# Performance work log

Measured on AMD Instinct MI355X. Metric: run time of the kernel, lower is better.

Reference implementation:

```python
import jax, jax.numpy as jnp
import numpy as np

N_NODES = 35
N_EDGES = 1190
N_VIEWS = 6
C1_IN, C1_OUT = 1, 256
C2_IN, C2_OUT = 256, 256
C3_IN, C3_OUT = 256, 64


def _nnconv(x, edge_attr, src, dst, nn_w, nn_b, lin_w, bias, c_in, c_out):
    """PyG NNConv with aggr='mean': per-edge MLP weight, gather-matvec-scatter."""
    # per-edge weight matrices: [E, c_in, c_out]
    W = jax.nn.relu(edge_attr @ nn_w.T + nn_b).reshape(-1, c_in, c_out)
    # gather source features and apply per-edge weight: [E, c_out]
    msg = jnp.einsum('ei,eio->eo', x[src], W)
    # scatter-mean into target nodes
    agg = jax.ops.segment_sum(msg, dst, num_segments=N_NODES)
    cnt = jax.ops.segment_sum(jnp.ones((msg.shape[0],), msg.dtype), dst,
                              num_segments=N_NODES)
    agg = agg / jnp.maximum(cnt, 1.0)[:, None]
    # root transform (lin has no bias in PyG) + conv bias
    return agg + x @ lin_w.T + bias


def setup_inputs() -> dict:
    key = jax.random.key(0)
    ks = jax.random.split(key, 16)
    s = 0.05
    x = jnp.ones((N_NODES, C1_IN), jnp.float32)
    edge_attr = jax.random.uniform(ks[0], (N_EDGES, N_VIEWS), jnp.float32)
    edge_index = jax.random.randint(ks[1], (2, N_EDGES), 0, N_NODES, jnp.int32)
    inp = {
        'x': x, 'edge_attr': edge_attr, 'edge_index': edge_index,
        'nn1_w': jax.random.normal(ks[2], (C1_IN * C1_OUT, N_VIEWS), jnp.float32) * s,
        'nn1_b': jax.random.normal(ks[3], (C1_IN * C1_OUT,), jnp.float32) * s,
        'lin1_w': jax.random.normal(ks[4], (C1_OUT, C1_IN), jnp.float32) * s,
        'b1': jax.random.normal(ks[5], (C1_OUT,), jnp.float32) * s,
        'nn2_w': jax.random.normal(ks[6], (C2_IN * C2_OUT, N_VIEWS), jnp.float32) * s,
        'nn2_b': jax.random.normal(ks[7], (C2_IN * C2_OUT,), jnp.float32) * s,
        'lin2_w': jax.random.normal(ks[8], (C2_OUT, C2_IN), jnp.float32) * s,
        'b2': jax.random.normal(ks[9], (C2_OUT,), jnp.float32) * s,
        'nn3_w': jax.random.normal(ks[10], (C3_IN * C3_OUT, N_VIEWS), jnp.float32) * s,
        'nn3_b': jax.random.normal(ks[11], (C3_IN * C3_OUT,), jnp.float32) * s,
        'lin3_w': jax.random.normal(ks[12], (C3_OUT, C3_IN), jnp.float32) * s,
        'b3': jax.random.normal(ks[13], (C3_OUT,), jnp.float32) * s,
    }
    return inp


def reference(x, edge_attr, edge_index, nn1_w, nn1_b, lin1_w, b1,
              nn2_w, nn2_b, lin2_w, b2, nn3_w, nn3_b, lin3_w, b3):
    src, dst = edge_index[0], edge_index[1]
    x = jax.nn.relu(_nnconv(x, edge_attr, src, dst, nn1_w, nn1_b, lin1_w, b1, C1_IN, C1_OUT))
    x = jax.nn.relu(_nnconv(x, edge_attr, src, dst, nn2_w, nn2_b, lin2_w, b2, C2_IN, C2_OUT))
    x = jax.nn.relu(_nnconv(x, edge_attr, src, dst, nn3_w, nn3_b, lin3_w, b3, C3_IN, C3_OUT))
    # CBT: pairwise L1 distances over feature dim -> [N, N]
    # (equivalent to repeat(35,1,1) / transpose / abs / sum since N == 35)
    cbt = jnp.abs(x[None, :, :] - x[:, None, :]).sum(-1)
    return cbt
```

## Files before the change

### kernel.cpp

```cpp
#include <hip/hip_runtime.h>


#define NN 35
#define NE 1190
#define MAXE 80

#define OFF_CNT  0
#define OFF_EL   64
#define OFF_X1   2944
#define OFF_X2   11904
#define OFF_X3   20864
#define OFF_AGG3 23168

__global__ __launch_bounds__(512) void x1_k(
    float* __restrict__ ws, const float* __restrict__ x,
    const float* __restrict__ ea, const int* __restrict__ ei,
    const float* __restrict__ w1, const float* __restrict__ b1w,
    const float* __restrict__ lin1, const float* __restrict__ b1) {
    __shared__ int elistS[MAXE];
    __shared__ int ecntS;
    __shared__ float partS[8 * 64];
    const int tid = threadIdx.x, bid = blockIdx.x;
    if (bid >= 140) {
        const int idx = (bid - 140) * 512 + tid;
        if (idx < NN * 64) ws[OFF_AGG3 + idx] = 0.f;
        return;
    }
    const int n = bid >> 2, och = bid & 3;
    if (tid == 0) ecntS = 0;
    __syncthreads();
    for (int e = tid; e < NE; e += 512) {
        if (ei[NE + e] == n) {
            const int p = atomicAdd(&ecntS, 1);
            if (p < MAXE) elistS[p] = e;
        }
    }
    __syncthreads();
    const int deg = ecntS;
    const int dl = deg < MAXE ? deg : MAXE;
    const int ol = tid & 63, ech = tid >> 6;
    const int o = och * 64 + ol;
    const float2* wr = (const float2*)(w1 + o * 6);
    const float2 wv0 = wr[0], wv1 = wr[1], wv2 = wr[2];
    const float bb = b1w[o];
    float a = 0.f;
    for (int k = ech; k < dl; k += 8) {
        const int e = elistS[k];
        const float2* eap = (const float2*)(ea + e * 6);
        const float2 a0 = eap[0], a1 = eap[1], a2 = eap[2];
        float d = bb;
        d = fmaf(a0.x, wv0.x, d); d = fmaf(a0.y, wv0.y, d);
        d = fmaf(a1.x, wv1.x, d); d = fmaf(a1.y, wv1.y, d);
        d = fmaf(a2.x, wv2.x, d); d = fmaf(a2.y, wv2.y, d);
        a = fmaf(x[ei[e]], fmaxf(d, 0.f), a);
    }
    partS[ech * 64 + ol] = a;
    __syncthreads();
    if (ech == 0) {
        float s = a;
#pragma unroll
        for (int p = 1; p < 8; p++) s += partS[p * 64 + ol];
        const float c = fmaxf((float)deg, 1.f);
        ws[OFF_X1 + n * 256 + o] = fmaxf(s / c + x[n] * lin1[o] + b1[o], 0.f);
    }
    if (och == 0) {
        if (tid < dl) ((int*)(ws + OFF_EL))[n * MAXE + tid] = elistS[tid];
        if (tid == 0) ws[OFF_CNT + n] = (float)deg;
    }
}

__global__ __launch_bounds__(512) void x2_k(
    float* __restrict__ ws, const float* __restrict__ ea,
    const int* __restrict__ ei, const float* __restrict__ w2,
    const float* __restrict__ b2w, const float* __restrict__ lin2,
    const float* __restrict__ b2) {
    __shared__ float smem[11264];
    float* xsS = smem;
    float* x1S = smem + 10240;
    float* easS = smem + 10496;
    int* srcS = (int*)(smem + 10976);
    int* elS = (int*)(smem + 11056);
    float* partA = smem;
    float* partB = smem + 512;
    __shared__ float cS;
    const int tid = threadIdx.x;
    const int n = blockIdx.x >> 4, og = blockIdx.x & 15;
    const int ol = tid & 15, ic = tid >> 4;
    const int o = og * 16 + ol;
    if (tid == 0) cS = ws[OFF_CNT + n];
    if (tid < MAXE) elS[tid] = ((const int*)(ws + OFF_EL))[n * MAXE + tid];
    if (tid >= 448) {
        const int q = tid - 448;
        *(float4*)&x1S[q * 4] = *(const float4*)(ws + OFF_X1 + n * 256 + q * 4);
    }
    __syncthreads();
    const int deg = (int)cS;
    const int dl = deg < MAXE ? deg : MAXE;
    if (tid < dl) {
        const int eid = elS[tid];
        srcS[tid] = ei[eid];
        const float2* eap = (const float2*)(ea + eid * 6);
        *(float2*)&easS[tid * 6] = eap[0];
        *(float2*)&easS[tid * 6 + 2] = eap[1];
        *(float2*)&easS[tid * 6 + 4] = eap[2];
    }
    float accm = 0.f;
    for (int p = 0; p < 2; ++p) {
        __syncthreads();
        for (int idx = tid; idx < dl * 32; idx += 512) {
            const int e = idx >> 5, ip = (idx & 31) * 4;
            *(float4*)&xsS[e * 128 + ip] =
                *(const float4*)(ws + OFF_X1 + srcS[e] * 256 + p * 128 + ip);
        }
        __syncthreads();
        const int i0 = p * 128 + ic * 4;
        const float* wp0 = w2 + (size_t)((i0 + 0) * 256 + o) * 6;
        const float* wp1 = w2 + (size_t)((i0 + 1) * 256 + o) * 6;
        const float* wp2 = w2 + (size_t)((i0 + 2) * 256 + o) * 6;
        const float* wp3 = w2 + (size_t)((i0 + 3) * 256 + o) * 6;
        const float2 wa0 = *(const float2*)wp0;
        const float2 wb0 = *(const float2*)(wp0 + 2);
        const float2 wc0 = *(const float2*)(wp0 + 4);
        const float2 wa1 = *(const float2*)wp1;
        const float2 wb1 = *(const float2*)(wp1 + 2);
        const float2 wc1 = *(const float2*)(wp1 + 4);
        const float2 wa2 = *(const float2*)wp2;
        const float2 wb2 = *(const float2*)(wp2 + 2);
        const float2 wc2 = *(const float2*)(wp2 + 4);
        const float2 wa3 = *(const float2*)wp3;
        const float2 wb3 = *(const float2*)(wp3 + 2);
        const float2 wc3 = *(const float2*)(wp3 + 4);
        const float bb0 = b2w[(i0 + 0) * 256 + o];
        const float bb1 = b2w[(i0 + 1) * 256 + o];
        const float bb2 = b2w[(i0 + 2) * 256 + o];
        const float bb3 = b2w[(i0 + 3) * 256 + o];
        for (int e = 0; e < dl; ++e) {
            const float2 e01 = *(const float2*)&easS[e * 6];
            const float2 e23 = *(const float2*)&easS[e * 6 + 2];
            const float2 e45 = *(const float2*)&easS[e * 6 + 4];
            const float4 xv = *(const float4*)&xsS[e * 128 + ic * 4];
            float d0 = bb0, d1 = bb1, d2 = bb2, d3 = bb3;
            d0 = fmaf(e01.x, wa0.x, d0); d1 = fmaf(e01.x, wa1.x, d1);
            d2 = fmaf(e01.x, wa2.x, d2); d3 = fmaf(e01.x, wa3.x, d3);
            d0 = fmaf(e01.y, wa0.y, d0); d1 = fmaf(e01.y, wa1.y, d1);
            d2 = fmaf(e01.y, wa2.y, d2); d3 = fmaf(e01.y, wa3.y, d3);
            d0 = fmaf(e23.x, wb0.x, d0); d1 = fmaf(e23.x, wb1.x, d1);
            d2 = fmaf(e23.x, wb2.x, d2); d3 = fmaf(e23.x, wb3.x, d3);
            d0 = fmaf(e23.y, wb0.y, d0); d1 = fmaf(e23.y, wb1.y, d1);
            d2 = fmaf(e23.y, wb2.y, d2); d3 = fmaf(e23.y, wb3.y, d3);
            d0 = fmaf(e45.x, wc0.x, d0); d1 = fmaf(e45.x, wc1.x, d1);
            d2 = fmaf(e45.x, wc2.x, d2); d3 = fmaf(e45.x, wc3.x, d3);
            d0 = fmaf(e45.y, wc0.y, d0); d1 = fmaf(e45.y, wc1.y, d1);
            d2 = fmaf(e45.y, wc2.y, d2); d3 = fmaf(e45.y, wc3.y, d3);
            d0 = fmaxf(d0, 0.f); d1 = fmaxf(d1, 0.f);
            d2 = fmaxf(d2, 0.f); d3 = fmaxf(d3, 0.f);
            accm = fmaf(xv.x, d0, accm);
            accm = fmaf(xv.y, d1, accm);
            accm = fmaf(xv.z, d2, accm);
            accm = fmaf(xv.w, d3, accm);
        }
    }
    float accl = 0.f;
    {
        const float4 l0 = *(const float4*)(lin2 + (size_t)o * 256 + ic * 4);
        const float4 xa = *(const float4*)&x1S[ic * 4];
        accl = fmaf(l0.x, xa.x, accl); accl = fmaf(l0.y, xa.y, accl);
        accl = fmaf(l0.z, xa.z, accl); accl = fmaf(l0.w, xa.w, accl);
        const float4 l1 = *(const float4*)(lin2 + (size_t)o * 256 + 128 + ic * 4);
        const float4 xb = *(const float4*)&x1S[128 + ic * 4];
        accl = fmaf(l1.x, xb.x, accl); accl = fmaf(l1.y, xb.y, accl);
        accl = fmaf(l1.z, xb.z, accl); accl = fmaf(l1.w, xb.w, accl);
    }
    __syncthreads();
    partA[ic * 16 + ol] = accm;
    partB[ic * 16 + ol] = accl;
    __syncthreads();
    if (tid < 16) {
        float m = 0.f, l = 0.f;
        for (int k = 0; k < 32; ++k) {
            m += partA[k * 16 + tid];
            l += partB[k * 16 + tid];
        }
        const float c = fmaxf(cS, 1.f);
        ws[OFF_X2 + n * 256 + og * 16 + tid] =
            fmaxf(m / c + l + b2[og * 16 + tid], 0.f);
    }
}

__global__ __launch_bounds__(512) void p3_k(
    float* __restrict__ ws, const float* __restrict__ ea,
    const int* __restrict__ ei, const float* __restrict__ w3,
    const float* __restrict__ b3w) {
    __shared__ float xsS[MAXE * 32];
    __shared__ float easS[MAXE * 6];
    __shared__ int srcS[MAXE];
    __shared__ int elS[MAXE];
    __shared__ float partS[8 * 64];
    __shared__ float cS;
    const int tid = threadIdx.x;
    const int n = blockIdx.x >> 3, iq = blockIdx.x & 7;
    const int i0 = iq * 32;
    const int ol = tid & 63, ic = tid >> 6;
    if (tid == 0) cS = ws[OFF_CNT + n];
    if (tid < MAXE) elS[tid] = ((const int*)(ws + OFF_EL))[n * MAXE + tid];
    __syncthreads();
    const int deg = (int)cS;
    const int dl = deg < MAXE ? deg : MAXE;
    if (tid < dl) {
        const int eid = elS[tid];
        srcS[tid] = ei[eid];
        const float2* eap = (const float2*)(ea + eid * 6);
        *(float2*)&easS[tid * 6] = eap[0];
        *(float2*)&easS[tid * 6 + 2] = eap[1];
        *(float2*)&easS[tid * 6 + 4] = eap[2];
    }
    __syncthreads();
    for (int idx = tid; idx < dl * 8; idx += 512) {
        const int e = idx >> 3, ip = (idx & 7) * 4;
        *(float4*)&xsS[e * 32 + ip] =
            *(const float4*)(ws + OFF_X2 + srcS[e] * 256 + i0 + ip);
    }
    __syncthreads();
    const int ib = i0 + ic * 4;
    const float* wp0 = w3 + (size_t)((ib + 0) * 64 + ol) * 6;
    const float* wp1 = w3 + (size_t)((ib + 1) * 64 + ol) * 6;
    const float* wp2 = w3 + (size_t)((ib + 2) * 64 + ol) * 6;
    const float* wp3 = w3 + (size_t)((ib + 3) * 64 + ol) * 6;
    const float2 wa0 = *(const float2*)wp0;
    const float2 wb0 = *(const float2*)(wp0 + 2);
    const float2 wc0 = *(const float2*)(wp0 + 4);
    const float2 wa1 = *(const float2*)wp1;
    const float2 wb1 = *(const float2*)(wp1 + 2);
    const float2 wc1 = *(const float2*)(wp1 + 4);
    const float2 wa2 = *(const float2*)wp2;
    const float2 wb2 = *(const float2*)(wp2 + 2);
    const float2 wc2 = *(const float2*)(wp2 + 4);
    const float2 wa3 = *(const float2*)wp3;
    const float2 wb3 = *(const float2*)(wp3 + 2);
    const float2 wc3 = *(const float2*)(wp3 + 4);
    const float bb0 = b3w[(ib + 0) * 64 + ol];
    const float bb1 = b3w[(ib + 1) * 64 + ol];
    const float bb2 = b3w[(ib + 2) * 64 + ol];
    const float bb3 = b3w[(ib + 3) * 64 + ol];
    float accm = 0.f;
    for (int e = 0; e < dl; ++e) {
        const float2 e01 = *(const float2*)&easS[e * 6];
        const float2 e23 = *(const float2*)&easS[e * 6 + 2];
        const float2 e45 = *(const float2*)&easS[e * 6 + 4];
        const float4 xv = *(const float4*)&xsS[e * 32 + ic * 4];
        float d0 = bb0, d1 = bb1, d2 = bb2, d3 = bb3;
        d0 = fmaf(e01.x, wa0.x, d0); d1 = fmaf(e01.x, wa1.x, d1);
        d2 = fmaf(e01.x, wa2.x, d2); d3 = fmaf(e01.x, wa3.x, d3);
        d0 = fmaf(e01.y, wa0.y, d0); d1 = fmaf(e01.y, wa1.y, d1);
        d2 = fmaf(e01.y, wa2.y, d2); d3 = fmaf(e01.y, wa3.y, d3);
        d0 = fmaf(e23.x, wb0.x, d0); d1 = fmaf(e23.x, wb1.x, d1);
        d2 = fmaf(e23.x, wb2.x, d2); d3 = fmaf(e23.x, wb3.x, d3);
        d0 = fmaf(e23.y, wb0.y, d0); d1 = fmaf(e23.y, wb1.y, d1);
        d2 = fmaf(e23.y, wb2.y, d2); d3 = fmaf(e23.y, wb3.y, d3);
        d0 = fmaf(e45.x, wc0.x, d0); d1 = fmaf(e45.x, wc1.x, d1);
        d2 = fmaf(e45.x, wc2.x, d2); d3 = fmaf(e45.x, wc3.x, d3);
        d0 = fmaf(e45.y, wc0.y, d0); d1 = fmaf(e45.y, wc1.y, d1);
        d2 = fmaf(e45.y, wc2.y, d2); d3 = fmaf(e45.y, wc3.y, d3);
        d0 = fmaxf(d0, 0.f); d1 = fmaxf(d1, 0.f);
        d2 = fmaxf(d2, 0.f); d3 = fmaxf(d3, 0.f);
        accm = fmaf(xv.x, d0, accm);
        accm = fmaf(xv.y, d1, accm);
        accm = fmaf(xv.z, d2, accm);
        accm = fmaf(xv.w, d3, accm);
    }
    partS[ic * 64 + ol] = accm;
    __syncthreads();
    if (ic == 0) {
        float s = accm;
#pragma unroll
        for (int p = 1; p < 8; ++p) s += partS[p * 64 + ol];
        atomicAdd(ws + OFF_AGG3 + n * 64 + ol, s);
    }
}

__global__ __launch_bounds__(256) void x3_k(float* __restrict__ ws,
                                            const float* __restrict__ lin3,
                                            const float* __restrict__ b3) {
    __shared__ float x2S[256];
    __shared__ float partS[3 * 64];
    __shared__ float cS;
    const int n = blockIdx.x, tid = threadIdx.x;
    const int o3 = tid & 63, ic = tid >> 6;
    if (tid == 0) cS = ws[OFF_CNT + n];
    if (tid < 64)
        *(float4*)&x2S[tid * 4] = *(const float4*)(ws + OFF_X2 + n * 256 + tid * 4);
    __syncthreads();
    const float4* l4 = (const float4*)(lin3 + (size_t)o3 * 256 + ic * 64);
    float s = 0.f;
#pragma unroll
    for (int k = 0; k < 16; k++) {
        const float4 wv = l4[k];
        const int i = ic * 64 + k * 4;
        s = fmaf(wv.x, x2S[i], s);
        s = fmaf(wv.y, x2S[i + 1], s);
        s = fmaf(wv.z, x2S[i + 2], s);
        s = fmaf(wv.w, x2S[i + 3], s);
    }
    if (ic > 0) partS[(ic - 1) * 64 + o3] = s;
    __syncthreads();
    if (ic == 0) {
        const float tot = s + partS[o3] + partS[64 + o3] + partS[128 + o3];
        const float c = fmaxf(cS, 1.f);
        ws[OFF_X3 + n * 64 + o3] =
            fmaxf(ws[OFF_AGG3 + n * 64 + o3] / c + tot + b3[o3], 0.f);
    }
}

__global__ __launch_bounds__(512) void cbt_k(const float* __restrict__ ws,
                                             float* __restrict__ out) {
    __shared__ float sx[NN * 64];
    const int tid = threadIdx.x;
    for (int idx = tid; idx < NN * 16; idx += 512)
        *(float4*)&sx[idx * 4] = *(const float4*)(ws + OFF_X3 + idx * 4);
    __syncthreads();
    const int f = tid & 63, jg = tid >> 6;
    const float xi = sx[blockIdx.x * 64 + f];
    for (int j = jg; j < NN; j += 8) {
        float d = fabsf(xi - sx[j * 64 + f]);
#pragma unroll
        for (int off = 32; off > 0; off >>= 1) d += __shfl_xor(d, off);
        if (f == 0) out[blockIdx.x * NN + j] = d;
    }
}

extern "C" void kernel_launch(void* const* d_in, const int* in_sizes, int n_in,
                              void* d_out, int out_size, void* d_ws, size_t ws_size,
                              hipStream_t stream) {
    (void)in_sizes; (void)n_in; (void)out_size; (void)ws_size;
    const float* x    = (const float*)d_in[0];
    const float* ea   = (const float*)d_in[1];
    const int*   ei   = (const int*)d_in[2];
    const float* nn1w = (const float*)d_in[3];
    const float* nn1b = (const float*)d_in[4];
    const float* lin1 = (const float*)d_in[5];
    const float* b1   = (const float*)d_in[6];
    const float* nn2w = (const float*)d_in[7];
    const float* nn2b = (const float*)d_in[8];
    const float* lin2 = (const float*)d_in[9];
    const float* b2   = (const float*)d_in[10];
    const float* nn3w = (const float*)d_in[11];
    const float* nn3b = (const float*)d_in[12];
    const float* lin3 = (const float*)d_in[13];
    const float* b3   = (const float*)d_in[14];

    float* ws = (float*)d_ws;
    x1_k<<<145, 512, 0, stream>>>(ws, x, ea, ei, nn1w, nn1b, lin1, b1);
    x2_k<<<NN * 16, 512, 0, stream>>>(ws, ea, ei, nn2w, nn2b, lin2, b2);
    p3_k<<<NN * 8, 512, 0, stream>>>(ws, ea, ei, nn3w, nn3b);
    x3_k<<<NN, 256, 0, stream>>>(ws, lin3, b3);
    cbt_k<<<NN, 512, 0, stream>>>(ws, (float*)d_out);
}
```

Baseline: 126.0 us.

## Fuse layer-3 root transform and CBT into p3 via last-block atomic counters

Merges the x3 and cbt kernels into the p3 kernel. Each node's eighth finishing block, detected with a per-node atomic counter, computes that node's layer-3 output. The globally last node block, detected with a done counter, then computes the full pairwise L1 distance matrix. This removes two kernel launches and their inter-kernel gaps. The cost is a serialized CBT tail in a single block, and a reliance on relaxed atomics with no explicit fences for cross-block visibility.

After: 166.7 us. 1.32x slower.

```diff
diff --git a/kernel.cpp b/kernel.cpp
--- a/kernel.cpp
+++ b/kernel.cpp
@@ -11,6 +11,15 @@
 #define OFF_X2   11904
 #define OFF_X3   20864
 #define OFF_AGG3 23168
+#define OFF_CNT3 25408
+#define OFF_DONE 25443
+
+__device__ __forceinline__ float ld_c(const float* p) {
+    return __hip_atomic_load(p, __ATOMIC_RELAXED, __HIP_MEMORY_SCOPE_AGENT);
+}
+__device__ __forceinline__ void st_c(float* p, float v) {
+    __hip_atomic_store(p, v, __ATOMIC_RELAXED, __HIP_MEMORY_SCOPE_AGENT);
+}
 
 __global__ __launch_bounds__(512) void x1_k(
     float* __restrict__ ws, const float* __restrict__ x,
@@ -23,7 +32,7 @@
     const int tid = threadIdx.x, bid = blockIdx.x;
     if (bid >= 140) {
         const int idx = (bid - 140) * 512 + tid;
-        if (idx < NN * 64) ws[OFF_AGG3 + idx] = 0.f;
+        if (idx < 2304) ws[OFF_AGG3 + idx] = 0.f;
         return;
     }
     const int n = bid >> 2, och = bid & 3;
@@ -187,16 +196,18 @@
     }
 }
 
-__global__ __launch_bounds__(512) void p3_k(
+__global__ __launch_bounds__(512) void p3c_k(
     float* __restrict__ ws, const float* __restrict__ ea,
     const int* __restrict__ ei, const float* __restrict__ w3,
-    const float* __restrict__ b3w) {
+    const float* __restrict__ b3w, const float* __restrict__ lin3,
+    const float* __restrict__ b3, float* __restrict__ out) {
     __shared__ float xsS[MAXE * 32];
     __shared__ float easS[MAXE * 6];
     __shared__ int srcS[MAXE];
     __shared__ int elS[MAXE];
     __shared__ float partS[8 * 64];
     __shared__ float cS;
+    __shared__ int roleS;
     const int tid = threadIdx.x;
     const int n = blockIdx.x >> 3, iq = blockIdx.x & 7;
     const int i0 = iq * 32;
@@ -276,55 +287,68 @@
         for (int p = 1; p < 8; ++p) s += partS[p * 64 + ol];
         atomicAdd(ws + OFF_AGG3 + n * 64 + ol, s);
     }
-}
-
-__global__ __launch_bounds__(256) void x3_k(float* __restrict__ ws,
-                                            const float* __restrict__ lin3,
-                                            const float* __restrict__ b3) {
-    __shared__ float x2S[256];
-    __shared__ float partS[3 * 64];
-    __shared__ float cS;
-    const int n = blockIdx.x, tid = threadIdx.x;
-    const int o3 = tid & 63, ic = tid >> 6;
-    if (tid == 0) cS = ws[OFF_CNT + n];
-    if (tid < 64)
-        *(float4*)&x2S[tid * 4] = *(const float4*)(ws + OFF_X2 + n * 256 + tid * 4);
-    __syncthreads();
-    const float4* l4 = (const float4*)(lin3 + (size_t)o3 * 256 + ic * 64);
-    float s = 0.f;
-#pragma unroll
-    for (int k = 0; k < 16; k++) {
-        const float4 wv = l4[k];
-        const int i = ic * 64 + k * 4;
-        s = fmaf(wv.x, x2S[i], s);
-        s = fmaf(wv.y, x2S[i + 1], s);
-        s = fmaf(wv.z, x2S[i + 2], s);
-        s = fmaf(wv.w, x2S[i + 3], s);
-    }
-    if (ic > 0) partS[(ic - 1) * 64 + o3] = s;
-    __syncthreads();
-    if (ic == 0) {
-        const float tot = s + partS[o3] + partS[64 + o3] + partS[128 + o3];
-        const float c = fmaxf(cS, 1.f);
-        ws[OFF_X3 + n * 64 + o3] =
-            fmaxf(ws[OFF_AGG3 + n * 64 + o3] / c + tot + b3[o3], 0.f);
-    }
-}
-
-__global__ __launch_bounds__(512) void cbt_k(const float* __restrict__ ws,
-                                             float* __restrict__ out) {
-    __shared__ float sx[NN * 64];
-    const int tid = threadIdx.x;
-    for (int idx = tid; idx < NN * 16; idx += 512)
-        *(float4*)&sx[idx * 4] = *(const float4*)(ws + OFF_X3 + idx * 4);
-    __syncthreads();
-    const int f = tid & 63, jg = tid >> 6;
-    const float xi = sx[blockIdx.x * 64 + f];
-    for (int j = jg; j < NN; j += 8) {
-        float d = fabsf(xi - sx[j * 64 + f]);
-#pragma unroll
-        for (int off = 32; off > 0; off >>= 1) d += __shfl_xor(d, off);
-        if (f == 0) out[blockIdx.x * NN + j] = d;
+    __syncthreads();
+    if (tid == 0) {
+        unsigned* cnt3 = (unsigned*)(ws + OFF_CNT3);
+        const unsigned old = __hip_atomic_fetch_add(
+            cnt3 + n, 1u, __ATOMIC_RELAXED, __HIP_MEMORY_SCOPE_AGENT);
+        roleS = (old == 7u);
+    }
+    __syncthreads();
+    if (!roleS) return;
+    {
+        float* x2S = xsS;
+        if (tid < 64)
+            *(float4*)&x2S[tid * 4] =
+                *(const float4*)(ws + OFF_X2 + n * 256 + tid * 4);
+        __syncthreads();
+        const int o3 = tid & 63, ic8 = tid >> 6;
+        const float4* l4 = (const float4*)(lin3 + (size_t)o3 * 256 + ic8 * 32);
+        const float* xs = x2S + ic8 * 32;
+        float s = 0.f;
+#pragma unroll
+        for (int k = 0; k < 8; k++) {
+            const float4 wv = l4[k];
+            s = fmaf(wv.x, xs[k * 4], s);
+            s = fmaf(wv.y, xs[k * 4 + 1], s);
+            s = fmaf(wv.z, xs[k * 4 + 2], s);
+            s = fmaf(wv.w, xs[k * 4 + 3], s);
+        }
+        partS[ic8 * 64 + o3] = s;
+        __syncthreads();
+        if (ic8 == 0) {
+            float t = s;
+#pragma unroll
+            for (int p = 1; p < 8; p++) t += partS[p * 64 + o3];
+            const float g = ld_c(ws + OFF_AGG3 + n * 64 + o3);
+            const float c = fmaxf(cS, 1.f);
+            st_c(ws + OFF_X3 + n * 64 + o3, fmaxf(g / c + t + b3[o3], 0.f));
+        }
+    }
+    __syncthreads();
+    if (tid == 0) {
+        unsigned* done = (unsigned*)(ws + OFF_DONE);
+        const unsigned old = __hip_atomic_fetch_add(
+            done, 1u, __ATOMIC_RELAXED, __HIP_MEMORY_SCOPE_AGENT);
+        roleS = (old == NN - 1u);
+    }
+    __syncthreads();
+    if (!roleS) return;
+    {
+        float* sx = xsS;
+        for (int idx = tid; idx < NN * 64; idx += 512)
+            sx[idx] = ld_c(ws + OFF_X3 + idx);
+        __syncthreads();
+        const int f = tid & 63, jg = tid >> 6;
+        for (int i = 0; i < NN; ++i) {
+            const float xi = sx[i * 64 + f];
+            for (int j = jg; j < NN; j += 8) {
+                float d = fabsf(xi - sx[j * 64 + f]);
+#pragma unroll
+                for (int off = 32; off > 0; off >>= 1) d += __shfl_xor(d, off);
+                if (f == 0) out[i * NN + j] = d;
+            }
+        }
     }
 }
 
@@ -351,7 +375,6 @@
     float* ws = (float*)d_ws;
     x1_k<<<145, 512, 0, stream>>>(ws, x, ea, ei, nn1w, nn1b, lin1, b1);
     x2_k<<<NN * 16, 512, 0, stream>>>(ws, ea, ei, nn2w, nn2b, lin2, b2);
-    p3_k<<<NN * 8, 512, 0, stream>>>(ws, ea, ei, nn3w, nn3b);
-    x3_k<<<NN, 256, 0, stream>>>(ws, lin3, b3);
-    cbt_k<<<NN, 512, 0, stream>>>(ws, (float*)d_out);
-}
+    p3c_k<<<NN * 8, 512, 0, stream>>>(ws, ea, ei, nn3w, nn3b, lin3, b3,
+                                      (float*)d_out);
+}
```

## Fuse layer-3 root transform and CBT distance into one single-block kernel

Applied to the files above, without the earlier changes.

Merges the x3 root-linear/finalize kernel and the pairwise L1 CBT kernel into a single kernel launched with one 512-thread block. It loads all of x2 into shared memory, computes x3 for every node, and then computes all 35x35 distances in the same block. This drops one launch and the global round trip for x3. In exchange, all of that work runs serially on a single CU instead of spread across 35 blocks.

Result: slower. 182.4 us (+44.8%).

```diff
diff --git a/kernel.cpp b/kernel.cpp
--- a/kernel.cpp
+++ b/kernel.cpp
@@ -9,7 +9,6 @@
 #define OFF_EL   64
 #define OFF_X1   2944
 #define OFF_X2   11904
-#define OFF_X3   20864
 #define OFF_AGG3 23168
 
 __global__ __launch_bounds__(512) void x1_k(
@@ -278,53 +277,89 @@
     }
 }
 
-__global__ __launch_bounds__(256) void x3_k(float* __restrict__ ws,
-                                            const float* __restrict__ lin3,
-                                            const float* __restrict__ b3) {
-    __shared__ float x2S[256];
-    __shared__ float partS[3 * 64];
-    __shared__ float cS;
-    const int n = blockIdx.x, tid = threadIdx.x;
-    const int o3 = tid & 63, ic = tid >> 6;
-    if (tid == 0) cS = ws[OFF_CNT + n];
-    if (tid < 64)
-        *(float4*)&x2S[tid * 4] = *(const float4*)(ws + OFF_X2 + n * 256 + tid * 4);
-    __syncthreads();
-    const float4* l4 = (const float4*)(lin3 + (size_t)o3 * 256 + ic * 64);
-    float s = 0.f;
+__global__ __launch_bounds__(512) void x3cbt_k(
+    const float* __restrict__ ws, const float* __restrict__ lin3,
+    const float* __restrict__ b3, float* __restrict__ out) {
+    __shared__ float x2S[NN * 256];
+    __shared__ float x3S[NN * 64];
+    const int tid = threadIdx.x;
+    for (int idx = tid; idx < NN * 64; idx += 512)
+        *(float4*)&x2S[idx * 4] = *(const float4*)(ws + OFF_X2 + idx * 4);
+    __syncthreads();
+    const int o3 = tid & 63, w = tid >> 6;
+    {
+        const float4* l4 = (const float4*)(lin3 + (size_t)o3 * 256);
+        float a0 = 0.f, a1 = 0.f, a2 = 0.f, a3 = 0.f, a4 = 0.f;
+        const bool has4 = (w + 32) < NN;
+        for (int k = 0; k < 64; ++k) {
+            const float4 wv = l4[k];
+            {
+                const float4 xv = *(const float4*)&x2S[w * 256 + k * 4];
+                a0 = fmaf(wv.x, xv.x, a0); a0 = fmaf(wv.y, xv.y, a0);
+                a0 = fmaf(wv.z, xv.z, a0); a0 = fmaf(wv.w, xv.w, a0);
+            }
+            {
+                const float4 xv = *(const float4*)&x2S[(w + 8) * 256 + k * 4];
+                a1 = fmaf(wv.x, xv.x, a1); a1 = fmaf(wv.y, xv.y, a1);
+                a1 = fmaf(wv.z, xv.z, a1); a1 = fmaf(wv.w, xv.w, a1);
+            }
+            {
+                const float4 xv = *(const float4*)&x2S[(w + 16) * 256 + k * 4];
+                a2 = fmaf(wv.x, xv.x, a2); a2 = fmaf(wv.y, xv.y, a2);
+                a2 = fmaf(wv.z, xv.z, a2); a2 = fmaf(wv.w, xv.w, a2);
+            }
+            {
+                const float4 xv = *(const float4*)&x2S[(w + 24) * 256 + k * 4];
+                a3 = fmaf(wv.x, xv.x, a3); a3 = fmaf(wv.y, xv.y, a3);
+                a3 = fmaf(wv.z, xv.z, a3); a3 = fmaf(wv.w, xv.w, a3);
+            }
+            if (has4) {
+                const float4 xv = *(const float4*)&x2S[(w + 32) * 256 + k * 4];
+                a4 = fmaf(wv.x, xv.x, a4); a4 = fmaf(wv.y, xv.y, a4);
+                a4 = fmaf(wv.z, xv.z, a4); a4 = fmaf(wv.w, xv.w, a4);
+            }
+        }
+        const float bb = b3[o3];
+        {
+            const int n = w;
+            const float c = fmaxf(ws[OFF_CNT + n], 1.f);
+            x3S[n * 64 + o3] =
+                fmaxf(ws[OFF_AGG3 + n * 64 + o3] / c + a0 + bb, 0.f);
+        }
+        {
+            const int n = w + 8;
+            const float c = fmaxf(ws[OFF_CNT + n], 1.f);
+            x3S[n * 64 + o3] =
+                fmaxf(ws[OFF_AGG3 + n * 64 + o3] / c + a1 + bb, 0.f);
+        }
+        {
+            const int n = w + 16;
+            const float c = fmaxf(ws[OFF_CNT + n], 1.f);
+            x3S[n * 64 + o3] =
+                fmaxf(ws[OFF_AGG3 + n * 64 + o3] / c + a2 + bb, 0.f);
+        }
+        {
+            const int n = w + 24;
+            const float c = fmaxf(ws[OFF_CNT + n], 1.f);
+            x3S[n * 64 + o3] =
+                fmaxf(ws[OFF_AGG3 + n * 64 + o3] / c + a3 + bb, 0.f);
+        }
+        if (has4) {
+            const int n = w + 32;
+            const float c = fmaxf(ws[OFF_CNT + n], 1.f);
+            x3S[n * 64 + o3] =
+                fmaxf(ws[OFF_AGG3 + n * 64 + o3] / c + a4 + bb, 0.f);
+        }
+    }
+    __syncthreads();
+    for (int i = 0; i < NN; ++i) {
+        const float xi = x3S[i * 64 + o3];
+        for (int j = w; j < NN; j += 8) {
+            float d = fabsf(xi - x3S[j * 64 + o3]);
 #pragma unroll
-    for (int k = 0; k < 16; k++) {
-        const float4 wv = l4[k];
-        const int i = ic * 64 + k * 4;
-        s = fmaf(wv.x, x2S[i], s);
-        s = fmaf(wv.y, x2S[i + 1], s);
-        s = fmaf(wv.z, x2S[i + 2], s);
-        s = fmaf(wv.w, x2S[i + 3], s);
-    }
-    if (ic > 0) partS[(ic - 1) * 64 + o3] = s;
-    __syncthreads();
-    if (ic == 0) {
-        const float tot = s + partS[o3] + partS[64 + o3] + partS[128 + o3];
-        const float c = fmaxf(cS, 1.f);
-        ws[OFF_X3 + n * 64 + o3] =
-            fmaxf(ws[OFF_AGG3 + n * 64 + o3] / c + tot + b3[o3], 0.f);
-    }
-}
-
-__global__ __launch_bounds__(512) void cbt_k(const float* __restrict__ ws,
-                                             float* __restrict__ out) {
-    __shared__ float sx[NN * 64];
-    const int tid = threadIdx.x;
-    for (int idx = tid; idx < NN * 16; idx += 512)
-        *(float4*)&sx[idx * 4] = *(const float4*)(ws + OFF_X3 + idx * 4);
-    __syncthreads();
-    const int f = tid & 63, jg = tid >> 6;
-    const float xi = sx[blockIdx.x * 64 + f];
-    for (int j = jg; j < NN; j += 8) {
-        float d = fabsf(xi - sx[j * 64 + f]);
-#pragma unroll
-        for (int off = 32; off > 0; off >>= 1) d += __shfl_xor(d, off);
-        if (f == 0) out[blockIdx.x * NN + j] = d;
+            for (int off = 32; off > 0; off >>= 1) d += __shfl_xor(d, off);
+            if (o3 == 0) out[i * NN + j] = d;
+        }
     }
 }
 
@@ -352,6 +387,5 @@
     x1_k<<<145, 512, 0, stream>>>(ws, x, ea, ei, nn1w, nn1b, lin1, b1);
     x2_k<<<NN * 16, 512, 0, stream>>>(ws, ea, ei, nn2w, nn2b, lin2, b2);
     p3_k<<<NN * 8, 512, 0, stream>>>(ws, ea, ei, nn3w, nn3b);
-    x3_k<<<NN, 256, 0, stream>>>(ws, lin3, b3);
-    cbt_k<<<NN, 512, 0, stream>>>(ws, (float*)d_out);
-}
+    x3cbt_k<<<1, 512, 0, stream>>>(ws, lin3, b3, (float*)d_out);
+}
```

## Fuse layer-3 message pass and root transform into one kernel without atomics

Applied to the files above, without the earlier changes.

Merges the layer-3 per-edge message kernel and the root-transform/finalize kernel into a single kernel. Each block now owns one node and 16 outputs and loops over all 256 inputs in two chunks. This removes the atomic accumulation buffer, its zeroing blocks in the first kernel, and one kernel launch. The trade-off is fewer blocks (140 instead of 280), each doing more sequential work per thread, and a larger shared-memory footprint.

Result: no change. 126.9 us (+0.8%).

```diff
diff --git a/kernel.cpp b/kernel.cpp
--- a/kernel.cpp
+++ b/kernel.cpp
@@ -10,7 +10,6 @@
 #define OFF_X1   2944
 #define OFF_X2   11904
 #define OFF_X3   20864
-#define OFF_AGG3 23168
 
 __global__ __launch_bounds__(512) void x1_k(
     float* __restrict__ ws, const float* __restrict__ x,
@@ -21,11 +20,6 @@
     __shared__ int ecntS;
     __shared__ float partS[8 * 64];
     const int tid = threadIdx.x, bid = blockIdx.x;
-    if (bid >= 140) {
-        const int idx = (bid - 140) * 512 + tid;
-        if (idx < NN * 64) ws[OFF_AGG3 + idx] = 0.f;
-        return;
-    }
     const int n = bid >> 2, och = bid & 3;
     if (tid == 0) ecntS = 0;
     __syncthreads();
@@ -187,22 +181,30 @@
     }
 }
 
-__global__ __launch_bounds__(512) void p3_k(
+__global__ __launch_bounds__(512) void p3x3_k(
     float* __restrict__ ws, const float* __restrict__ ea,
     const int* __restrict__ ei, const float* __restrict__ w3,
-    const float* __restrict__ b3w) {
-    __shared__ float xsS[MAXE * 32];
-    __shared__ float easS[MAXE * 6];
-    __shared__ int srcS[MAXE];
-    __shared__ int elS[MAXE];
-    __shared__ float partS[8 * 64];
+    const float* __restrict__ b3w, const float* __restrict__ lin3,
+    const float* __restrict__ b3) {
+    __shared__ float smem[11264];
+    float* xsS = smem;
+    float* x2S = smem + 10240;
+    float* easS = smem + 10496;
+    int* srcS = (int*)(smem + 10976);
+    int* elS = (int*)(smem + 11056);
+    float* partA = smem;
+    float* partB = smem + 512;
     __shared__ float cS;
     const int tid = threadIdx.x;
-    const int n = blockIdx.x >> 3, iq = blockIdx.x & 7;
-    const int i0 = iq * 32;
-    const int ol = tid & 63, ic = tid >> 6;
+    const int n = blockIdx.x >> 2, og = blockIdx.x & 3;
+    const int ol = tid & 15, ic = tid >> 4;
+    const int o = og * 16 + ol;
     if (tid == 0) cS = ws[OFF_CNT + n];
     if (tid < MAXE) elS[tid] = ((const int*)(ws + OFF_EL))[n * MAXE + tid];
+    if (tid >= 448) {
+        const int q = tid - 448;
+        *(float4*)&x2S[q * 4] = *(const float4*)(ws + OFF_X2 + n * 256 + q * 4);
+    }
     __syncthreads();
     const int deg = (int)cS;
     const int dl = deg < MAXE ? deg : MAXE;
@@ -214,100 +216,86 @@
         *(float2*)&easS[tid * 6 + 2] = eap[1];
         *(float2*)&easS[tid * 6 + 4] = eap[2];
     }
-    __syncthreads();
-    for (int idx = tid; idx < dl * 8; idx += 512) {
-        const int e = idx >> 3, ip = (idx & 7) * 4;
-        *(float4*)&xsS[e * 32 + ip] =
-            *(const float4*)(ws + OFF_X2 + srcS[e] * 256 + i0 + ip);
-    }
-    __syncthreads();
-    const int ib = i0 + ic * 4;
-    const float* wp0 = w3 + (size_t)((ib + 0) * 64 + ol) * 6;
-    const float* wp1 = w3 + (size_t)((ib + 1) * 64 + ol) * 6;
-    const float* wp2 = w3 + (size_t)((ib + 2) * 64 + ol) * 6;
-    const float* wp3 = w3 + (size_t)((ib + 3) * 64 + ol) * 6;
-    const float2 wa0 = *(const float2*)wp0;
-    const float2 wb0 = *(const float2*)(wp0 + 2);
-    const float2 wc0 = *(const float2*)(wp0 + 4);
-    const float2 wa1 = *(const float2*)wp1;
-    const float2 wb1 = *(const float2*)(wp1 + 2);
-    const float2 wc1 = *(const float2*)(wp1 + 4);
-    const float2 wa2 = *(const float2*)wp2;
-    const float2 wb2 = *(const float2*)(wp2 + 2);
-    const float2 wc2 = *(const float2*)(wp2 + 4);
-    const float2 wa3 = *(const float2*)wp3;
-    const float2 wb3 = *(const float2*)(wp3 + 2);
-    const float2 wc3 = *(const float2*)(wp3 + 4);
-    const float bb0 = b3w[(ib + 0) * 64 + ol];
-    const float bb1 = b3w[(ib + 1) * 64 + ol];
-    const float bb2 = b3w[(ib + 2) * 64 + ol];
-    const float bb3 = b3w[(ib + 3) * 64 + ol];
     float accm = 0.f;
-    for (int e = 0; e < dl; ++e) {
-        const float2 e01 = *(const float2*)&easS[e * 6];
-        const float2 e23 = *(const float2*)&easS[e * 6 + 2];
-        const float2 e45 = *(const float2*)&easS[e * 6 + 4];
-        const float4 xv = *(const float4*)&xsS[e * 32 + ic * 4];
-        float d0 = bb0, d1 = bb1, d2 = bb2, d3 = bb3;
-        d0 = fmaf(e01.x, wa0.x, d0); d1 = fmaf(e01.x, wa1.x, d1);
-        d2 = fmaf(e01.x, wa2.x, d2); d3 = fmaf(e01.x, wa3.x, d3);
-        d0 = fmaf(e01.y, wa0.y, d0); d1 = fmaf(e01.y, wa1.y, d1);
-        d2 = fmaf(e01.y, wa2.y, d2); d3 = fmaf(e01.y, wa3.y, d3);
-        d0 = fmaf(e23.x, wb0.x, d0); d1 = fmaf(e23.x, wb1.x, d1);
-        d2 = fmaf(e23.x, wb2.x, d2); d3 = fmaf(e23.x, wb3.x, d3);
-        d0 = fmaf(e23.y, wb0.y, d0); d1 = fmaf(e23.y, wb1.y, d1);
-        d2 = fmaf(e23.y, wb2.y, d2); d3 = fmaf(e23.y, wb3.y, d3);
-        d0 = fmaf(e45.x, wc0.x, d0); d1 = fmaf(e45.x, wc1.x, d1);
-        d2 = fmaf(e45.x, wc2.x, d2); d3 = fmaf(e45.x, wc3.x, d3);
-        d0 = fmaf(e45.y, wc0.y, d0); d1 = fmaf(e45.y, wc1.y, d1);
-        d2 = fmaf(e45.y, wc2.y, d2); d3 = fmaf(e45.y, wc3.y, d3);
-        d0 = fmaxf(d0, 0.f); d1 = fmaxf(d1, 0.f);
-        d2 = fmaxf(d2, 0.f); d3 = fmaxf(d3, 0.f);
-        accm = fmaf(xv.x, d0, accm);
-        accm = fmaf(xv.y, d1, accm);
-        accm = fmaf(xv.z, d2, accm);
-        accm = fmaf(xv.w, d3, accm);
-    }
-    partS[ic * 64 + ol] = accm;
-    __syncthreads();
-    if (ic == 0) {
-        float s = accm;
-#pragma unroll
-        for (int p = 1; p < 8; ++p) s += partS[p * 64 + ol];
-        atomicAdd(ws + OFF_AGG3 + n * 64 + ol, s);
-    }
-}
-
-__global__ __launch_bounds__(256) void x3_k(float* __restrict__ ws,
-                                            const float* __restrict__ lin3,
-                                            const float* __restrict__ b3) {
-    __shared__ float x2S[256];
-    __shared__ float partS[3 * 64];
-    __shared__ float cS;
-    const int n = blockIdx.x, tid = threadIdx.x;
-    const int o3 = tid & 63, ic = tid >> 6;
-    if (tid == 0) cS = ws[OFF_CNT + n];
-    if (tid < 64)
-        *(float4*)&x2S[tid * 4] = *(const float4*)(ws + OFF_X2 + n * 256 + tid * 4);
-    __syncthreads();
-    const float4* l4 = (const float4*)(lin3 + (size_t)o3 * 256 + ic * 64);
-    float s = 0.f;
-#pragma unroll
-    for (int k = 0; k < 16; k++) {
-        const float4 wv = l4[k];
-        const int i = ic * 64 + k * 4;
-        s = fmaf(wv.x, x2S[i], s);
-        s = fmaf(wv.y, x2S[i + 1], s);
-        s = fmaf(wv.z, x2S[i + 2], s);
-        s = fmaf(wv.w, x2S[i + 3], s);
-    }
-    if (ic > 0) partS[(ic - 1) * 64 + o3] = s;
-    __syncthreads();
-    if (ic == 0) {
-        const float tot = s + partS[o3] + partS[64 + o3] + partS[128 + o3];
+    for (int p = 0; p < 2; ++p) {
+        __syncthreads();
+        for (int idx = tid; idx < dl * 32; idx += 512) {
+            const int e = idx >> 5, ip = (idx & 31) * 4;
+            *(float4*)&xsS[e * 128 + ip] =
+                *(const float4*)(ws + OFF_X2 + srcS[e] * 256 + p * 128 + ip);
+        }
+        __syncthreads();
+        const int i0 = p * 128 + ic * 4;
+        const float* wp0 = w3 + (size_t)((i0 + 0) * 64 + o) * 6;
+        const float* wp1 = w3 + (size_t)((i0 + 1) * 64 + o) * 6;
+        const float* wp2 = w3 + (size_t)((i0 + 2) * 64 + o) * 6;
+        const float* wp3 = w3 + (size_t)((i0 + 3) * 64 + o) * 6;
+        const float2 wa0 = *(const float2*)wp0;
+        const float2 wb0 = *(const float2*)(wp0 + 2);
+        const float2 wc0 = *(const float2*)(wp0 + 4);
+        const float2 wa1 = *(const float2*)wp1;
+        const float2 wb1 = *(const float2*)(wp1 + 2);
+        const float2 wc1 = *(const float2*)(wp1 + 4);
+        const float2 wa2 = *(const float2*)wp2;
+        const float2 wb2 = *(const float2*)(wp2 + 2);
+        const float2 wc2 = *(const float2*)(wp2 + 4);
+        const float2 wa3 = *(const float2*)wp3;
+        const float2 wb3 = *(const float2*)(wp3 + 2);
+        const float2 wc3 = *(const float2*)(wp3 + 4);
+        const float bb0 = b3w[(i0 + 0) * 64 + o];
+        const float bb1 = b3w[(i0 + 1) * 64 + o];
+        const float bb2 = b3w[(i0 + 2) * 64 + o];
+        const float bb3 = b3w[(i0 + 3) * 64 + o];
+        for (int e = 0; e < dl; ++e) {
+            const float2 e01 = *(const float2*)&easS[e * 6];
+            const float2 e23 = *(const float2*)&easS[e * 6 + 2];
+            const float2 e45 = *(const float2*)&easS[e * 6 + 4];
+            const float4 xv = *(const float4*)&xsS[e * 128 + ic * 4];
+            float d0 = bb0, d1 = bb1, d2 = bb2, d3 = bb3;
+            d0 = fmaf(e01.x, wa0.x, d0); d1 = fmaf(e01.x, wa1.x, d1);
+            d2 = fmaf(e01.x, wa2.x, d2); d3 = fmaf(e01.x, wa3.x, d3);
+            d0 = fmaf(e01.y, wa0.y, d0); d1 = fmaf(e01.y, wa1.y, d1);
+            d2 = fmaf(e01.y, wa2.y, d2); d3 = fmaf(e01.y, wa3.y, d3);
+            d0 = fmaf(e23.x, wb0.x, d0); d1 = fmaf(e23.x, wb1.x, d1);
+            d2 = fmaf(e23.x, wb2.x, d2); d3 = fmaf(e23.x, wb3.x, d3);
+            d0 = fmaf(e23.y, wb0.y, d0); d1 = fmaf(e23.y, wb1.y, d1);
+            d2 = fmaf(e23.y, wb2.y, d2); d3 = fmaf(e23.y, wb3.y, d3);
+            d0 = fmaf(e45.x, wc0.x, d0); d1 = fmaf(e45.x, wc1.x, d1);
+            d2 = fmaf(e45.x, wc2.x, d2); d3 = fmaf(e45.x, wc3.x, d3);
+            d0 = fmaf(e45.y, wc0.y, d0); d1 = fmaf(e45.y, wc1.y, d1);
+            d2 = fmaf(e45.y, wc2.y, d2); d3 = fmaf(e45.y, wc3.y, d3);
+            d0 = fmaxf(d0, 0.f); d1 = fmaxf(d1, 0.f);
+            d2 = fmaxf(d2, 0.f); d3 = fmaxf(d3, 0.f);
+            accm = fmaf(xv.x, d0, accm);
+            accm = fmaf(xv.y, d1, accm);
+            accm = fmaf(xv.z, d2, accm);
+            accm = fmaf(xv.w, d3, accm);
+        }
+    }
+    float accl = 0.f;
+    {
+        const float4 l0 = *(const float4*)(lin3 + (size_t)o * 256 + ic * 4);
+        const float4 xa = *(const float4*)&x2S[ic * 4];
+        accl = fmaf(l0.x, xa.x, accl); accl = fmaf(l0.y, xa.y, accl);
+        accl = fmaf(l0.z, xa.z, accl); accl = fmaf(l0.w, xa.w, accl);
+        const float4 l1 = *(const float4*)(lin3 + (size_t)o * 256 + 128 + ic * 4);
+        const float4 xb = *(const float4*)&x2S[128 + ic * 4];
+        accl = fmaf(l1.x, xb.x, accl); accl = fmaf(l1.y, xb.y, accl);
+        accl = fmaf(l1.z, xb.z, accl); accl = fmaf(l1.w, xb.w, accl);
+    }
+    __syncthreads();
+    partA[ic * 16 + ol] = accm;
+    partB[ic * 16 + ol] = accl;
+    __syncthreads();
+    if (tid < 16) {
+        float m = 0.f, l = 0.f;
+        for (int k = 0; k < 32; ++k) {
+            m += partA[k * 16 + tid];
+            l += partB[k * 16 + tid];
+        }
         const float c = fmaxf(cS, 1.f);
-        ws[OFF_X3 + n * 64 + o3] =
-            fmaxf(ws[OFF_AGG3 + n * 64 + o3] / c + tot + b3[o3], 0.f);
+        ws[OFF_X3 + n * 64 + og * 16 + tid] =
+            fmaxf(m / c + l + b3[og * 16 + tid], 0.f);
     }
 }
 
@@ -349,9 +337,8 @@
     const float* b3   = (const float*)d_in[14];
 
     float* ws = (float*)d_ws;
-    x1_k<<<145, 512, 0, stream>>>(ws, x, ea, ei, nn1w, nn1b, lin1, b1);
+    x1_k<<<140, 512, 0, stream>>>(ws, x, ea, ei, nn1w, nn1b, lin1, b1);
     x2_k<<<NN * 16, 512, 0, stream>>>(ws, ea, ei, nn2w, nn2b, lin2, b2);
-    p3_k<<<NN * 8, 512, 0, stream>>>(ws, ea, ei, nn3w, nn3b);
-    x3_k<<<NN, 256, 0, stream>>>(ws, lin3, b3);
+    p3x3_k<<<NN * 4, 512, 0, stream>>>(ws, ea, ei, nn3w, nn3b, lin3, b3);
     cbt_k<<<NN, 512, 0, stream>>>(ws, (float*)d_out);
 }
```
